# Kernel tuning notes

Hardware: AMD Instinct MI355X
Metric: run time of the kernel (lower is better)

The kernel has to match this reference:

```python
import jax, jax.numpy as jnp
import numpy as np

DIM = 1024
HEADS = 16
B, N = 4, 1024

def setup_inputs() -> dict:
    key = jax.random.key(0)
    k1, k2, k3 = jax.random.split(key, 3)
    x = jax.random.normal(k1, (B, N, DIM), dtype=jnp.float32)
    # xavier-uniform-ish init scale
    Wqkv = jax.random.normal(k2, (3 * DIM, DIM), dtype=jnp.float32) * (1.0 / np.sqrt(DIM))
    bqkv = jnp.zeros((3 * DIM,), dtype=jnp.float32)
    W1 = jax.random.normal(k3, (DIM, DIM), dtype=jnp.float32) * (1.0 / np.sqrt(DIM))
    b1 = jnp.zeros((DIM,), dtype=jnp.float32)
    return {"x": x, "Wqkv": Wqkv, "bqkv": bqkv, "W1": W1, "b1": b1}

def reference(x, Wqkv, bqkv, W1, b1):
    b, n, dim = x.shape
    h = HEADS
    d = dim // h
    scale = dim ** (-0.5)  # NOTE: module scales by full dim, not head dim
    qkv = x @ Wqkv.T + bqkv  # [b, n, 3*dim]
    qkv = qkv.reshape(b, n, 3, h, d)
    q = jnp.transpose(qkv[:, :, 0], (0, 2, 1, 3))  # [b, h, n, d]
    k = jnp.transpose(qkv[:, :, 1], (0, 2, 1, 3))
    v = jnp.transpose(qkv[:, :, 2], (0, 2, 1, 3))
    dots = jnp.einsum('bhid,bhjd->bhij', q, k) * scale
    attn = jax.nn.softmax(dots, axis=-1)
    out = jnp.einsum('bhij,bhjd->bhid', attn, v)
    out = jnp.transpose(out, (0, 2, 1, 3)).reshape(b, n, dim)
    out = out @ W1.T + b1
    return out
```

## Files before the change

### kernel.cpp

```cpp
#include <hip/hip_runtime.h>
#include <cmath>

typedef __bf16 bf16;
typedef __bf16 bf16x8 __attribute__((ext_vector_type(8)));
typedef __bf16 bf16x4 __attribute__((ext_vector_type(4)));
typedef float f32x4 __attribute__((ext_vector_type(4)));

#define MFMA16(a, b, c) __builtin_amdgcn_mfma_f32_16x16x32_bf16(a, b, c, 0, 0, 0)

__device__ __forceinline__ void load_lds16(const void* g, void* l) {
    __builtin_amdgcn_global_load_lds(
        (const __attribute__((address_space(1))) void*)g,
        (__attribute__((address_space(3))) void*)l, 16, 0, 0);
}

__device__ __forceinline__ bf16x8 load8(const bf16* p) { return *(const bf16x8*)p; }
__device__ __forceinline__ bf16x8 load8(const float* p) {
    float4 f0 = *(const float4*)p;
    float4 f1 = *(const float4*)(p + 4);
    bf16x8 r;
    r[0] = (bf16)f0.x; r[1] = (bf16)f0.y; r[2] = (bf16)f0.z; r[3] = (bf16)f0.w;
    r[4] = (bf16)f1.x; r[5] = (bf16)f1.y; r[6] = (bf16)f1.z; r[7] = (bf16)f1.w;
    return r;
}

__global__ __launch_bounds__(256) void cvt3(
    const float* __restrict__ s0, bf16* __restrict__ d0, int n0,
    const float* __restrict__ s1, bf16* __restrict__ d1, int n1,
    const float* __restrict__ s2, bf16* __restrict__ d2, int n2)
{
    int i = blockIdx.x * 256 + threadIdx.x;
    const float* s; bf16* d; int base;
    if (i < n0)                { s = s0; d = d0; base = i; }
    else if (i < n0 + n1)      { s = s1; d = d1; base = i - n0; }
    else if (i < n0 + n1 + n2) { s = s2; d = d2; base = i - n0 - n1; }
    else return;
    *(bf16x8*)(d + (size_t)base * 8) = load8(s + (size_t)base * 8);
}

template <int EPI, typename TB, int BN>
__global__ __launch_bounds__(256) void gemm_bt(
    const bf16* __restrict__ A, const TB* __restrict__ Bm,
    const float* __restrict__ bias,
    bf16* __restrict__ qo, bf16* __restrict__ ko, bf16* __restrict__ vto,
    float* __restrict__ C, int M, int N, int K)
{
    constexpr int WN = BN / 2;
    constexpr int JN = WN / 16;
    constexpr int SLOTS = (128 + BN) * 8;

    __shared__ bf16 As[128 * 64];
    __shared__ bf16 Bs[BN * 64];

    const int tid = threadIdx.x;
    const int l   = tid & 63;
    const int w   = tid >> 6;
    const int wm  = w & 1, wn = w >> 1;
    const int l15 = l & 15;
    const int g   = l >> 4;
    const int swz = l15 & 7;
    const int m0  = blockIdx.y * 128;
    const int n0  = blockIdx.x * BN;

    f32x4 acc[4][JN] = {};

    for (int k0 = 0; k0 < K; k0 += 64) {
        __syncthreads();
        #pragma unroll
        for (int it = 0; it < SLOTS / 256; ++it) {
            int s = it * 256 + w * 64 + l;
            if (s < 1024) {
                int row = s >> 3, pc = s & 7;
                int lc  = pc ^ (row & 7);
                load_lds16(A + (size_t)(m0 + row) * K + k0 + lc * 8, &As[s * 8]);
            } else {
                int t = s - 1024;
                int row = t >> 3, pc = t & 7;
                int lc  = pc ^ (row & 7);
                if constexpr (sizeof(TB) == 2) {
                    load_lds16(Bm + (size_t)(n0 + row) * K + k0 + lc * 8, &Bs[t * 8]);
                } else {
                    *(bf16x8*)&Bs[t * 8] = load8(Bm + (size_t)(n0 + row) * K + k0 + lc * 8);
                }
            }
        }
        __syncthreads();
        #pragma unroll
        for (int kk = 0; kk < 64; kk += 32) {
            bf16x8 aF[4], bF[JN];
            #pragma unroll
            for (int i = 0; i < 4; ++i)
                aF[i] = *(const bf16x8*)&As[(wm * 64 + i * 16 + l15) * 64
                                            + ((((kk >> 3) + g) ^ swz) * 8)];
            #pragma unroll
            for (int j = 0; j < JN; ++j)
                bF[j] = *(const bf16x8*)&Bs[(wn * WN + j * 16 + l15) * 64
                                            + ((((kk >> 3) + g) ^ swz) * 8)];
            #pragma unroll
            for (int i = 0; i < 4; ++i)
                #pragma unroll
                for (int j = 0; j < JN; ++j)
                    acc[i][j] = MFMA16(aF[i], bF[j], acc[i][j]);
        }
    }

    #pragma unroll
    for (int j = 0; j < JN; ++j) {
        int gcol = n0 + wn * WN + j * 16 + l15;
        float bv = bias[gcol];
        if (EPI == 0) {
            int which = gcol >> 10;
            int h  = (gcol >> 6) & 15;
            int dd = gcol & 63;
            #pragma unroll
            for (int i = 0; i < 4; ++i) {
                #pragma unroll
                for (int r = 0; r < 4; ++r) {
                    int grow = m0 + wm * 64 + i * 16 + g * 4 + r;
                    int b    = grow >> 10;
                    int npos = grow & 1023;
                    float v  = acc[i][j][r] + bv;
                    size_t bh = (size_t)(b * 16 + h);
                    if (which == 0)
                        qo[(bh * 1024 + npos) * 64 + dd] = (bf16)v;
                    else if (which == 1)
                        ko[(bh * 1024 + npos) * 64 + dd] = (bf16)v;
                    else
                        vto[(bh * 64 + dd) * 1024 + npos] = (bf16)v;
                }
            }
        } else {
            #pragma unroll
            for (int i = 0; i < 4; ++i)
                #pragma unroll
                for (int r = 0; r < 4; ++r) {
                    int grow = m0 + wm * 64 + i * 16 + g * 4 + r;
                    C[(size_t)grow * N + gcol] = acc[i][j][r] + bv;
                }
        }
    }
}

__global__ __launch_bounds__(256) void attn_fused(
    const bf16* __restrict__ qb, const bf16* __restrict__ kb,
    const bf16* __restrict__ vtb, bf16* __restrict__ attn)
{
    __shared__ bf16 Ks[2][64 * 64];
    __shared__ bf16 Vts[2][64 * 64];
    __shared__ bf16 Ps[4][2][16][40];

    const int tid = threadIdx.x;
    const int l   = tid & 63;
    const int w   = tid >> 6;
    const int l15 = l & 15;
    const int g   = l >> 4;
    const int swz = l15 & 7;
    const int bid = blockIdx.x;
    const int bh  = bid & 63;
    const int qc  = bid >> 6;
    const int m0  = qc * 128;

    const bf16* q_bh  = qb  + (size_t)bh * 65536;
    const bf16* k_bh  = kb  + (size_t)bh * 65536;
    const bf16* vt_bh = vtb + (size_t)bh * 65536;

    bf16x8 qf[2][2];
    #pragma unroll
    for (int qg = 0; qg < 2; ++qg)
        #pragma unroll
        for (int kk = 0; kk < 2; ++kk)
            qf[qg][kk] = *(const bf16x8*)(q_bh
                + (size_t)(m0 + w * 32 + qg * 16 + l15) * 64 + kk * 32 + g * 8);

    f32x4 o[2][4] = {};
    float lsum[2] = {0.f, 0.f};

    const float C_EXP = 0.04508422f;

    auto stage = [&](int buf, int j0) {
        #pragma unroll
        for (int it = 0; it < 2; ++it) {
            int s   = it * 256 + w * 64 + l;
            int row = s >> 3, pc = s & 7;
            int lc  = pc ^ (row & 7);
            load_lds16(k_bh + (size_t)(j0 + row) * 64 + lc * 8, &Ks[buf][s * 8]);
            load_lds16(vt_bh + (size_t)row * 1024 + j0 + lc * 8, &Vts[buf][s * 8]);
        }
    };

    stage(0, 0);

    for (int t = 0; t < 16; ++t) {
        const int c = t & 1;
        __syncthreads();
        if (t < 15) stage(c ^ 1, (t + 1) * 64);

        f32x4 s4[2][4] = {};
        #pragma unroll
        for (int kk = 0; kk < 2; ++kk) {
            bf16x8 kf[4];
            #pragma unroll
            for (int js = 0; js < 4; ++js)
                kf[js] = *(const bf16x8*)&Ks[c][(js * 16 + l15) * 64
                                                + (((kk * 4 + g) ^ swz) * 8)];
            __builtin_amdgcn_s_setprio(1);
            #pragma unroll
            for (int qg = 0; qg < 2; ++qg)
                #pragma unroll
                for (int js = 0; js < 4; ++js)
                    s4[qg][js] = MFMA16(kf[js], qf[qg][kk], s4[qg][js]);
            __builtin_amdgcn_s_setprio(0);
        }

        #pragma unroll
        for (int h = 0; h < 2; ++h) {
            #pragma unroll
            for (int qg = 0; qg < 2; ++qg) {
                #pragma unroll
                for (int jsl = 0; jsl < 2; ++jsl) {
                    int js = h * 2 + jsl;
                    bf16x4 pk;
                    float ps = 0.f;
                    #pragma unroll
                    for (int r = 0; r < 4; ++r) {
                        float p = exp2f(s4[qg][js][r] * C_EXP);
                        ps += p;
                        pk[r] = (bf16)p;
                    }
                    lsum[qg] += ps;
                    *(bf16x4*)&Ps[w][qg][l15][jsl * 16 + g * 4] = pk;
                }
            }
            bf16x8 vf[4];
            #pragma unroll
            for (int ns = 0; ns < 4; ++ns)
                vf[ns] = *(const bf16x8*)&Vts[c][(ns * 16 + l15) * 64
                                                 + (((h * 4 + g) ^ swz) * 8)];
            __builtin_amdgcn_s_setprio(1);
            #pragma unroll
            for (int qg = 0; qg < 2; ++qg) {
                bf16x8 pf = *(const bf16x8*)&Ps[w][qg][l15][g * 8];
                #pragma unroll
                for (int ns = 0; ns < 4; ++ns)
                    o[qg][ns] = MFMA16(pf, vf[ns], o[qg][ns]);
            }
            __builtin_amdgcn_s_setprio(0);
        }
    }

    float tden[2];
    #pragma unroll
    for (int qg = 0; qg < 2; ++qg) {
        float t = lsum[qg];
        t += __shfl_xor(t, 16);
        t += __shfl_xor(t, 32);
        tden[qg] = t;
    }

    #pragma unroll
    for (int qg = 0; qg < 2; ++qg) {
        #pragma unroll
        for (int r = 0; r < 4; ++r) {
            float inv = 1.0f / __shfl(tden[qg], g * 4 + r);
            int grow = m0 + w * 32 + qg * 16 + g * 4 + r;
            size_t obase = ((size_t)(bh >> 4) * 1024 + grow) * 1024 + (bh & 15) * 64;
            #pragma unroll
            for (int ns = 0; ns < 4; ++ns)
                attn[obase + ns * 16 + l15] = (bf16)(o[qg][ns][r] * inv);
        }
    }
}

extern "C" void kernel_launch(void* const* d_in, const int* in_sizes, int n_in,
                              void* d_out, int out_size, void* d_ws, size_t ws_size,
                              hipStream_t stream)
{
    const float* x    = (const float*)d_in[0];
    const float* Wqkv = (const float*)d_in[1];
    const float* bqkv = (const float*)d_in[2];
    const float* W1   = (const float*)d_in[3];
    const float* b1   = (const float*)d_in[4];
    float* out = (float*)d_out;

    const size_t SEG = (size_t)4 * 16 * 1024 * 64;
    bf16* xbf  = (bf16*)d_ws;
    bf16* qb   = xbf + SEG;
    bf16* kb   = qb + SEG;
    bf16* vtb  = kb + SEG;
    bf16* attnb = xbf;
    bf16* wqkvbf = vtb + SEG;
    bf16* w1bf   = wqkvbf + 3145728;

    const bool cw = ws_size >= (size_t)(5 * SEG) * sizeof(bf16);

    const int nx = 524288;
    const int nw = cw ? 393216 : 0;
    const int n1 = cw ? 131072 : 0;
    const int tot = nx + nw + n1;
    cvt3<<<dim3((tot + 255) / 256), 256, 0, stream>>>(
        x, xbf, nx, Wqkv, wqkvbf, nw, W1, w1bf, n1);

    if (cw)
        gemm_bt<0, bf16, 128><<<dim3(24, 32), 256, 0, stream>>>(
            xbf, wqkvbf, bqkv, qb, kb, vtb, nullptr, 4096, 3072, 1024);
    else
        gemm_bt<0, float, 128><<<dim3(24, 32), 256, 0, stream>>>(
            xbf, Wqkv, bqkv, qb, kb, vtb, nullptr, 4096, 3072, 1024);

    attn_fused<<<dim3(512), 256, 0, stream>>>(qb, kb, vtb, attnb);

    if (cw)
        gemm_bt<1, bf16, 64><<<dim3(16, 32), 256, 0, stream>>>(
            attnb, w1bf, b1, nullptr, nullptr, nullptr, out, 4096, 1024, 1024);
    else
        gemm_bt<1, float, 64><<<dim3(16, 32), 256, 0, stream>>>(
            attnb, W1, b1, nullptr, nullptr, nullptr, out, 4096, 1024, 1024);
}
```

Measured before the change: 173.6 us.

## Split attention KV tiles across two wave groups and vectorize V-transpose stores

The attention kernel now runs 512 threads per block. Two groups of four waves each process half of every 64-key tile, and their partial outputs and denominators are reduced through LDS at the end. This doubles the number of waves available to hide latency, at the cost of an extra reduction pass and two block barriers. The Ps scratch buffer is XOR-swizzled to avoid LDS bank conflicts, and the QKV GEMM epilogue writes the transposed V as 4-element vectors instead of scalar stores.

Result: faster. 167.7 us (-3.4%).

```diff
diff --git a/kernel.cpp b/kernel.cpp
--- a/kernel.cpp
+++ b/kernel.cpp
@@ -112,21 +112,34 @@
             int which = gcol >> 10;
             int h  = (gcol >> 6) & 15;
             int dd = gcol & 63;
-            #pragma unroll
-            for (int i = 0; i < 4; ++i) {
-                #pragma unroll
-                for (int r = 0; r < 4; ++r) {
-                    int grow = m0 + wm * 64 + i * 16 + g * 4 + r;
-                    int b    = grow >> 10;
-                    int npos = grow & 1023;
-                    float v  = acc[i][j][r] + bv;
+            if (which == 2) {
+                #pragma unroll
+                for (int i = 0; i < 4; ++i) {
+                    int grow0 = m0 + wm * 64 + i * 16 + g * 4;
+                    int b     = grow0 >> 10;
+                    int npos  = grow0 & 1023;
                     size_t bh = (size_t)(b * 16 + h);
-                    if (which == 0)
-                        qo[(bh * 1024 + npos) * 64 + dd] = (bf16)v;
-                    else if (which == 1)
-                        ko[(bh * 1024 + npos) * 64 + dd] = (bf16)v;
-                    else
-                        vto[(bh * 64 + dd) * 1024 + npos] = (bf16)v;
+                    bf16x4 pv;
+                    #pragma unroll
+                    for (int r = 0; r < 4; ++r)
+                        pv[r] = (bf16)(acc[i][j][r] + bv);
+                    *(bf16x4*)&vto[(bh * 64 + dd) * 1024 + npos] = pv;
+                }
+            } else {
+                #pragma unroll
+                for (int i = 0; i < 4; ++i) {
+                    #pragma unroll
+                    for (int r = 0; r < 4; ++r) {
+                        int grow = m0 + wm * 64 + i * 16 + g * 4 + r;
+                        int b    = grow >> 10;
+                        int npos = grow & 1023;
+                        float v  = acc[i][j][r] + bv;
+                        size_t bh = (size_t)(b * 16 + h);
+                        if (which == 0)
+                            qo[(bh * 1024 + npos) * 64 + dd] = (bf16)v;
+                        else
+                            ko[(bh * 1024 + npos) * 64 + dd] = (bf16)v;
+                    }
                 }
             }
         } else {
@@ -141,17 +154,19 @@
     }
 }
 
-__global__ __launch_bounds__(256) void attn_fused(
+__global__ __launch_bounds__(512, 4) void attn_fused(
     const bf16* __restrict__ qb, const bf16* __restrict__ kb,
     const bf16* __restrict__ vtb, bf16* __restrict__ attn)
 {
     __shared__ bf16 Ks[2][64 * 64];
     __shared__ bf16 Vts[2][64 * 64];
-    __shared__ bf16 Ps[4][2][16][40];
+    __shared__ bf16 Ps[8][2][16][32];
 
     const int tid = threadIdx.x;
     const int l   = tid & 63;
     const int w   = tid >> 6;
+    const int wq  = w & 3;
+    const int wh  = w >> 2;
     const int l15 = l & 15;
     const int g   = l >> 4;
     const int swz = l15 & 7;
@@ -170,7 +185,7 @@
         #pragma unroll
         for (int kk = 0; kk < 2; ++kk)
             qf[qg][kk] = *(const bf16x8*)(q_bh
-                + (size_t)(m0 + w * 32 + qg * 16 + l15) * 64 + kk * 32 + g * 8);
+                + (size_t)(m0 + wq * 32 + qg * 16 + l15) * 64 + kk * 32 + g * 8);
 
     f32x4 o[2][4] = {};
     float lsum[2] = {0.f, 0.f};
@@ -178,14 +193,11 @@
     const float C_EXP = 0.04508422f;
 
     auto stage = [&](int buf, int j0) {
-        #pragma unroll
-        for (int it = 0; it < 2; ++it) {
-            int s   = it * 256 + w * 64 + l;
-            int row = s >> 3, pc = s & 7;
-            int lc  = pc ^ (row & 7);
-            load_lds16(k_bh + (size_t)(j0 + row) * 64 + lc * 8, &Ks[buf][s * 8]);
-            load_lds16(vt_bh + (size_t)row * 1024 + j0 + lc * 8, &Vts[buf][s * 8]);
-        }
+        int s   = tid;
+        int row = s >> 3, pc = s & 7;
+        int lc  = pc ^ (row & 7);
+        load_lds16(k_bh + (size_t)(j0 + row) * 64 + lc * 8, &Ks[buf][s * 8]);
+        load_lds16(vt_bh + (size_t)row * 1024 + j0 + lc * 8, &Vts[buf][s * 8]);
     };
 
     stage(0, 0);
@@ -195,57 +207,55 @@
         __syncthreads();
         if (t < 15) stage(c ^ 1, (t + 1) * 64);
 
-        f32x4 s4[2][4] = {};
+        f32x4 s4[2][2] = {};
         #pragma unroll
         for (int kk = 0; kk < 2; ++kk) {
-            bf16x8 kf[4];
-            #pragma unroll
-            for (int js = 0; js < 4; ++js)
-                kf[js] = *(const bf16x8*)&Ks[c][(js * 16 + l15) * 64
-                                                + (((kk * 4 + g) ^ swz) * 8)];
+            bf16x8 kf[2];
+            #pragma unroll
+            for (int jsl = 0; jsl < 2; ++jsl)
+                kf[jsl] = *(const bf16x8*)&Ks[c][((wh * 2 + jsl) * 16 + l15) * 64
+                                                 + (((kk * 4 + g) ^ swz) * 8)];
             __builtin_amdgcn_s_setprio(1);
             #pragma unroll
             for (int qg = 0; qg < 2; ++qg)
                 #pragma unroll
-                for (int js = 0; js < 4; ++js)
-                    s4[qg][js] = MFMA16(kf[js], qf[qg][kk], s4[qg][js]);
+                for (int jsl = 0; jsl < 2; ++jsl)
+                    s4[qg][jsl] = MFMA16(kf[jsl], qf[qg][kk], s4[qg][jsl]);
             __builtin_amdgcn_s_setprio(0);
         }
 
         #pragma unroll
-        for (int h = 0; h < 2; ++h) {
-            #pragma unroll
-            for (int qg = 0; qg < 2; ++qg) {
-                #pragma unroll
-                for (int jsl = 0; jsl < 2; ++jsl) {
-                    int js = h * 2 + jsl;
-                    bf16x4 pk;
-                    float ps = 0.f;
-                    #pragma unroll
-                    for (int r = 0; r < 4; ++r) {
-                        float p = exp2f(s4[qg][js][r] * C_EXP);
-                        ps += p;
-                        pk[r] = (bf16)p;
-                    }
-                    lsum[qg] += ps;
-                    *(bf16x4*)&Ps[w][qg][l15][jsl * 16 + g * 4] = pk;
-                }
+        for (int qg = 0; qg < 2; ++qg) {
+            #pragma unroll
+            for (int jsl = 0; jsl < 2; ++jsl) {
+                bf16x4 pk;
+                float ps = 0.f;
+                #pragma unroll
+                for (int r = 0; r < 4; ++r) {
+                    float p = exp2f(s4[qg][jsl][r] * C_EXP);
+                    ps += p;
+                    pk[r] = (bf16)p;
+                }
+                lsum[qg] += ps;
+                *(bf16x4*)&Ps[w][qg][l15][(((jsl * 2 + (g >> 1)) ^ (l15 & 3)) * 8)
+                                          + (g & 1) * 4] = pk;
             }
-            bf16x8 vf[4];
+        }
+
+        bf16x8 vf[4];
+        #pragma unroll
+        for (int ns = 0; ns < 4; ++ns)
+            vf[ns] = *(const bf16x8*)&Vts[c][(ns * 16 + l15) * 64
+                                             + (((wh * 4 + g) ^ swz) * 8)];
+        __builtin_amdgcn_s_setprio(1);
+        #pragma unroll
+        for (int qg = 0; qg < 2; ++qg) {
+            bf16x8 pf = *(const bf16x8*)&Ps[w][qg][l15][(g ^ (l15 & 3)) * 8];
             #pragma unroll
             for (int ns = 0; ns < 4; ++ns)
-                vf[ns] = *(const bf16x8*)&Vts[c][(ns * 16 + l15) * 64
-                                                 + (((h * 4 + g) ^ swz) * 8)];
-            __builtin_amdgcn_s_setprio(1);
-            #pragma unroll
-            for (int qg = 0; qg < 2; ++qg) {
-                bf16x8 pf = *(const bf16x8*)&Ps[w][qg][l15][g * 8];
-                #pragma unroll
-                for (int ns = 0; ns < 4; ++ns)
-                    o[qg][ns] = MFMA16(pf, vf[ns], o[qg][ns]);
-            }
-            __builtin_amdgcn_s_setprio(0);
-        }
+                o[qg][ns] = MFMA16(pf, vf[ns], o[qg][ns]);
+        }
+        __builtin_amdgcn_s_setprio(0);
     }
 
     float tden[2];
@@ -257,16 +267,41 @@
         tden[qg] = t;
     }
 
-    #pragma unroll
-    for (int qg = 0; qg < 2; ++qg) {
-        #pragma unroll
-        for (int r = 0; r < 4; ++r) {
-            float inv = 1.0f / __shfl(tden[qg], g * 4 + r);
-            int grow = m0 + w * 32 + qg * 16 + g * 4 + r;
-            size_t obase = ((size_t)(bh >> 4) * 1024 + grow) * 1024 + (bh & 15) * 64;
-            #pragma unroll
-            for (int ns = 0; ns < 4; ++ns)
-                attn[obase + ns * 16 + l15] = (bf16)(o[qg][ns][r] * inv);
+    float* R0 = (float*)&Ks[0][0];
+    float* R1 = (float*)&Vts[0][0];
+    float* DN = (float*)&Ps[0][0][0][0];
+    __syncthreads();
+    if (wh == 1) {
+        #pragma unroll
+        for (int ns = 0; ns < 4; ++ns) {
+            *(f32x4*)&R0[((wq * 64 + l) * 4 + ns) * 4] = o[0][ns];
+            *(f32x4*)&R1[((wq * 64 + l) * 4 + ns) * 4] = o[1][ns];
+        }
+        DN[(wq * 2 + 0) * 64 + l] = tden[0];
+        DN[(wq * 2 + 1) * 64 + l] = tden[1];
+    }
+    __syncthreads();
+    if (wh == 0) {
+        #pragma unroll
+        for (int ns = 0; ns < 4; ++ns) {
+            o[0][ns] += *(const f32x4*)&R0[((wq * 64 + l) * 4 + ns) * 4];
+            o[1][ns] += *(const f32x4*)&R1[((wq * 64 + l) * 4 + ns) * 4];
+        }
+        tden[0] += DN[(wq * 2 + 0) * 64 + l];
+        tden[1] += DN[(wq * 2 + 1) * 64 + l];
+
+        #pragma unroll
+        for (int qg = 0; qg < 2; ++qg) {
+            #pragma unroll
+            for (int r = 0; r < 4; ++r) {
+                float inv = 1.0f / __shfl(tden[qg], g * 4 + r);
+                int grow = m0 + wq * 32 + qg * 16 + g * 4 + r;
+                size_t obase = ((size_t)(bh >> 4) * 1024 + grow) * 1024
+                               + (bh & 15) * 64;
+                #pragma unroll
+                for (int ns = 0; ns < 4; ++ns)
+                    attn[obase + ns * 16 + l15] = (bf16)(o[qg][ns][r] * inv);
+            }
         }
     }
 }
@@ -307,7 +342,7 @@
         gemm_bt<0, float, 128><<<dim3(24, 32), 256, 0, stream>>>(
             xbf, Wqkv, bqkv, qb, kb, vtb, nullptr, 4096, 3072, 1024);
 
-    attn_fused<<<dim3(512), 256, 0, stream>>>(qb, kb, vtb, attnb);
+    attn_fused<<<dim3(512), 512, 0, stream>>>(qb, kb, vtb, attnb);
 
     if (cw)
         gemm_bt<1, bf16, 64><<<dim3(16, 32), 256, 0, stream>>>(
```
